# Performance work log

Hardware: AMD Instinct MI355X
Metric: run time of the kernel (lower is better)

## Reference

```python
import jax, jax.numpy as jnp
import numpy as np

B, S, D = 4, 2048, 2048
E = 8
H = (4 * D) // E  # per-expert hidden = 1024
DS = D // 2       # shared-layer hidden
LOAD_BALANCE_WEIGHT = 0.01


def setup_inputs() -> dict:
    key = jax.random.key(0)
    ks = jax.random.split(key, 12)
    s = 0.02
    return {
        "x": jax.random.normal(ks[0], (B, S, D), dtype=jnp.float32),
        "W_router": jax.random.normal(ks[1], (D, E), dtype=jnp.float32) * s,
        "b_router": jnp.zeros((E,), dtype=jnp.float32),
        "W1": jax.random.normal(ks[2], (E, D, H), dtype=jnp.float32) * s,
        "b1": jnp.zeros((E, H), dtype=jnp.float32),
        "W2": jax.random.normal(ks[3], (E, H, D), dtype=jnp.float32) * s,
        "b2": jnp.zeros((E, D), dtype=jnp.float32),
        "Ws1": jax.random.normal(ks[4], (D, DS), dtype=jnp.float32) * s,
        "bs1": jnp.zeros((DS,), dtype=jnp.float32),
        "Ws2": jax.random.normal(ks[5], (DS, D), dtype=jnp.float32) * s,
        "bs2": jnp.zeros((D,), dtype=jnp.float32),
    }


def reference(x, W_router, b_router, W1, b1, W2, b2, Ws1, bs1, Ws2, bs2):
    # Router: soft weights over all experts (soft-MoE, every expert runs).
    router_logits = jnp.einsum("bsd,de->bse", x, W_router) + b_router
    router_weights = jax.nn.softmax(router_logits, axis=-1)  # (B,S,E)

    # Shared branch: Linear -> GELU (exact, matching torch default) -> Linear.
    shared = jax.nn.gelu(jnp.einsum("bsd,dh->bsh", x, Ws1) + bs1, approximate=False)
    shared = jnp.einsum("bsh,hd->bsd", shared, Ws2) + bs2

    # All experts as one batched GEMM pair (fuses the torch Python loop).
    h = jax.nn.gelu(jnp.einsum("bsd,edh->bseh", x, W1) + b1, approximate=False)  # (B,S,E,H)
    expert_out = jnp.einsum("bseh,ehd->bsed", h, W2) + b2  # (B,S,E,D)

    # Softmax-weighted combine + scaled shared residual (dropout=0 / eval).
    weighted = jnp.einsum("bsed,bse->bsd", expert_out, router_weights)
    output = weighted + 0.1 * shared

    # Load-balance aux loss: MSE between mean usage and uniform.
    expert_usage = router_weights.mean(axis=(0, 1))  # (E,)
    uniform = jnp.full_like(expert_usage, 1.0 / E)
    aux_loss = jnp.mean((expert_usage - uniform) ** 2) * LOAD_BALANCE_WEIGHT
    return output, aux_loss
```

## Files before the change

kernel.cpp:

```cpp
#include <hip/hip_runtime.h>
#include <hip/hip_bf16.h>
#include <stdint.h>

#define DEV static __device__ __forceinline__

typedef __attribute__((ext_vector_type(4))) float f32x4;
typedef __attribute__((ext_vector_type(8))) short bf16x8;
typedef __attribute__((ext_vector_type(4))) float float4v;

constexpr int NBATCH = 4;
constexpr int SEQ    = 2048;
constexpr int DIM    = 2048;
constexpr int NEXP   = 8;
constexpr int HEXP   = 1024;
constexpr int DSH    = 1024;
constexpr int NTOK   = NBATCH * SEQ;
constexpr int JEXP   = NEXP * HEXP;
constexpr int JTOT   = JEXP + DSH;

DEV short f2bf(float f) {
  __hip_bfloat16 b = __float2bfloat16(f);
  union { __hip_bfloat16 b; short s; } u; u.b = b; return u.s;
}

DEV void gload16(const void* gp, const void* lp) {
  __builtin_amdgcn_global_load_lds(
      (__attribute__((address_space(1))) void*)(uintptr_t)gp,
      (__attribute__((address_space(3))) void*)(uint32_t)(uintptr_t)lp,
      16, 0, 0);
}

__global__ void conv_x_k(const float* __restrict__ x, short* __restrict__ xb) {
  size_t i = (size_t)blockIdx.x * blockDim.x + threadIdx.x;
  const float4v* s = reinterpret_cast<const float4v*>(x) + i * 2;
  float4v a = s[0], b = s[1];
  bf16x8 o;
  o[0] = f2bf(a.x); o[1] = f2bf(a.y); o[2] = f2bf(a.z); o[3] = f2bf(a.w);
  o[4] = f2bf(b.x); o[5] = f2bf(b.y); o[6] = f2bf(b.z); o[7] = f2bf(b.w);
  *reinterpret_cast<bf16x8*>(xb + i * 8) = o;
}

__global__ __launch_bounds__(256) void router_k(
    const float* __restrict__ x, const float* __restrict__ Wr,
    const float* __restrict__ br, float* __restrict__ rw,
    float* __restrict__ auxs) {
  const int wave = threadIdx.x >> 6, lane = threadIdx.x & 63;
  const int t = blockIdx.x * 4 + wave;
  const float* xr = x + (size_t)t * DIM;
  float a[NEXP];
#pragma unroll
  for (int e = 0; e < NEXP; ++e) a[e] = 0.f;
  for (int i = 0; i < DIM / 64; ++i) {
    int k = i * 64 + lane;
    float xv = xr[k];
    const float* w = Wr + (size_t)k * NEXP;
#pragma unroll
    for (int e = 0; e < NEXP; ++e) a[e] = fmaf(xv, w[e], a[e]);
  }
#pragma unroll
  for (int e = 0; e < NEXP; ++e) {
    float v = a[e];
#pragma unroll
    for (int off = 32; off > 0; off >>= 1) v += __shfl_xor(v, off, 64);
    a[e] = v + br[e];
  }
  float mx = a[0];
#pragma unroll
  for (int e = 1; e < NEXP; ++e) mx = fmaxf(mx, a[e]);
  float s = 0.f;
#pragma unroll
  for (int e = 0; e < NEXP; ++e) { a[e] = expf(a[e] - mx); s += a[e]; }
  float inv = 1.f / s;
#pragma unroll
  for (int e = 0; e < NEXP; ++e) a[e] *= inv;
  if (lane == 0) {
#pragma unroll
    for (int e = 0; e < NEXP; ++e) rw[(size_t)t * NEXP + e] = a[e];
  }
  __shared__ float blk[NEXP];
  if (threadIdx.x < NEXP) blk[threadIdx.x] = 0.f;
  __syncthreads();
  if (lane == 0) {
#pragma unroll
    for (int e = 0; e < NEXP; ++e) atomicAdd(&blk[e], a[e]);
  }
  __syncthreads();
  if (threadIdx.x < NEXP) atomicAdd(&auxs[threadIdx.x], blk[threadIdx.x]);
}

__global__ void zero_aux_k(float* auxs) {
  if (threadIdx.x < NEXP) auxs[threadIdx.x] = 0.f;
}

__global__ void fin_aux_k(const float* __restrict__ auxs, float* __restrict__ dst) {
  if (threadIdx.x == 0) {
    float s = 0.f;
    for (int e = 0; e < NEXP; ++e) {
      float u = auxs[e] / (float)NTOK - (1.0f / NEXP);
      s += u * u;
    }
    dst[0] = (s / NEXP) * 0.01f;
  }
}

__global__ __launch_bounds__(256) void conv_w1_k(
    const float* __restrict__ W1, const float* __restrict__ Ws1,
    short* __restrict__ dst, int jbase, int jc) {
  __shared__ float tile[64][65];
  const int j0 = jbase + blockIdx.x * 64;
  const int k0 = blockIdx.y * 64;
  const int tx = threadIdx.x & 63;
  const int ty = threadIdx.x >> 6;
#pragma unroll
  for (int i = 0; i < 16; ++i) {
    int kk = ty * 16 + i;
    int j = j0 + tx, k = k0 + kk;
    float v;
    if (j < JEXP) {
      int e = j >> 10, h = j & 1023;
      v = W1[(size_t)e * DIM * HEXP + (size_t)k * HEXP + h];
    } else {
      v = Ws1[(size_t)k * DSH + (j - JEXP)];
    }
    tile[kk][tx] = v;
  }
  __syncthreads();
#pragma unroll
  for (int i = 0; i < 16; ++i) {
    int jj = ty * 16 + i;
    int jloc = j0 - jbase + jj;
    dst[(size_t)jloc * DIM + k0 + tx] = f2bf(tile[tx][jj]);
  }
}

__global__ __launch_bounds__(256) void conv_w2_k(
    const float* __restrict__ W2, const float* __restrict__ Ws2,
    short* __restrict__ dst, int jbase, int jc) {
  __shared__ float tile[64][65];
  const int j0 = jbase + blockIdx.x * 64;
  const int d0 = blockIdx.y * 64;
  const int tx = threadIdx.x & 63;
  const int ty = threadIdx.x >> 6;
#pragma unroll
  for (int i = 0; i < 16; ++i) {
    int jj = ty * 16 + i;
    int j = j0 + jj;
    float v;
    if (j < JEXP) {
      int e = j >> 10, h = j & 1023;
      v = W2[(size_t)e * HEXP * DIM + (size_t)h * DIM + d0 + tx];
    } else {
      v = 0.1f * Ws2[(size_t)(j - JEXP) * DIM + d0 + tx];
    }
    tile[jj][tx] = v;
  }
  __syncthreads();
#pragma unroll
  for (int i = 0; i < 16; ++i) {
    int dd = ty * 16 + i;
    dst[(size_t)(d0 + dd) * jc + (j0 - jbase) + tx] = f2bf(tile[tx][dd]);
  }
}

#define MF_ROW(MI, AV)                                                           \
  acc[MI][0] = __builtin_amdgcn_mfma_f32_16x16x32_bf16(AV, b0, acc[MI][0], 0, 0, 0); \
  acc[MI][1] = __builtin_amdgcn_mfma_f32_16x16x32_bf16(AV, b1, acc[MI][1], 0, 0, 0); \
  acc[MI][2] = __builtin_amdgcn_mfma_f32_16x16x32_bf16(AV, b2, acc[MI][2], 0, 0, 0); \
  acc[MI][3] = __builtin_amdgcn_mfma_f32_16x16x32_bf16(AV, b3, acc[MI][3], 0, 0, 0);

template <int MODE>
__global__ __launch_bounds__(512, 2) void gemm256(
    const short* __restrict__ A, const short* __restrict__ Bt, int K,
    const float* __restrict__ rw,
    const float* __restrict__ bias_a, const float* __restrict__ bias_b,
    short* __restrict__ hOut, int jbase, int jc,
    float* __restrict__ out, int nx) {
  extern __shared__ short smem[];
  short* As = smem;
  short* Bs = smem + 32768;

  const int tid = threadIdx.x;
  const int w = tid >> 6, lane = tid & 63;
  const int wr = w >> 2, wc = w & 3;

  const int nwg = nx * (NTOK / 256);
  int orig = blockIdx.x;
  const int q = nwg >> 3, r = nwg & 7;
  const int xcd = orig & 7, off = orig >> 3;
  const int bid = (xcd < r ? xcd * (q + 1) : r * (q + 1) + (xcd - r) * q) + off;
  const int bx = bid % nx, by = bid / nx;
  const int m0 = by * 256, n0 = bx * 256;

  f32x4 acc[8][4] = {};

  const int aoff = ((lane & 15) << 6) + ((((lane >> 4) ^ ((lane >> 1) & 3)) & 3) << 4);
  const char* Abase = (const char*)As + wr * 8192 + aoff;
  const char* Bbase = (const char*)Bs + wc * 4096 + aoff;

  const int srow = lane >> 2;
  const int scol = (((lane & 3) ^ ((lane >> 3) & 3)) << 3);
  const short* gA0 = A + (size_t)(m0 + w * 32 + srow) * K + scol;
  const short* gB0 = Bt + (size_t)(n0 + w * 32 + srow) * K + scol;
  const size_t k16 = (size_t)16 * K;
  short* lA = As + w * 1024;
  short* lB = Bs + w * 1024;
  const int NT = K >> 5;

#define STG_A(TT) { const int sl_ = (TT) & 3; const size_t co_ = (size_t)(TT) << 5; \
    gload16(gA0 + co_, lA + sl_ * 8192);                                           \
    gload16(gA0 + k16 + co_, lA + sl_ * 8192 + 512); }
#define STG_B(TT) { const int sl_ = (TT) & 3; const size_t co_ = (size_t)(TT) << 5; \
    gload16(gB0 + co_, lB + sl_ * 8192);                                           \
    gload16(gB0 + k16 + co_, lB + sl_ * 8192 + 512); }

  STG_A(0); STG_B(0); STG_A(1); STG_B(1); STG_A(2); STG_B(2);
  asm volatile("s_waitcnt vmcnt(8)" ::: "memory");
  __builtin_amdgcn_s_barrier();

  for (int t = 0; t < NT; ++t) {
    const char* pa = Abase + (size_t)(t & 3) * 16384;
    const char* pb = Bbase + (size_t)(t & 3) * 16384;
    bf16x8 b0 = *(const bf16x8*)(pb);
    bf16x8 b1 = *(const bf16x8*)(pb + 1024);
    bf16x8 b2 = *(const bf16x8*)(pb + 2048);
    bf16x8 b3 = *(const bf16x8*)(pb + 3072);
    bf16x8 a0 = *(const bf16x8*)(pa);
    bf16x8 a1 = *(const bf16x8*)(pa + 1024);
    bf16x8 a2 = *(const bf16x8*)(pa + 2048);
    bf16x8 a3 = *(const bf16x8*)(pa + 3072);
    if (t + 3 < NT) STG_A(t + 3);
    __builtin_amdgcn_s_barrier();
    asm volatile("s_waitcnt lgkmcnt(0)" ::: "memory");
    __builtin_amdgcn_sched_barrier(0);
    __builtin_amdgcn_s_setprio(1);
    MF_ROW(0, a0) MF_ROW(1, a1) MF_ROW(2, a2) MF_ROW(3, a3)
    __builtin_amdgcn_s_setprio(0);
    __builtin_amdgcn_s_barrier();
    a0 = *(const bf16x8*)(pa + 4096);
    a1 = *(const bf16x8*)(pa + 5120);
    a2 = *(const bf16x8*)(pa + 6144);
    a3 = *(const bf16x8*)(pa + 7168);
    if (t + 3 < NT) STG_B(t + 3);
    __builtin_amdgcn_s_barrier();
    asm volatile("s_waitcnt lgkmcnt(0)" ::: "memory");
    __builtin_amdgcn_sched_barrier(0);
    __builtin_amdgcn_s_setprio(1);
    MF_ROW(4, a0) MF_ROW(5, a1) MF_ROW(6, a2) MF_ROW(7, a3)
    __builtin_amdgcn_s_setprio(0);
    if (t <= NT - 4)      { asm volatile("s_waitcnt vmcnt(8)" ::: "memory"); }
    else if (t == NT - 3) { asm volatile("s_waitcnt vmcnt(4)" ::: "memory"); }
    else if (t == NT - 2) { asm volatile("s_waitcnt vmcnt(0)" ::: "memory"); }
    __builtin_amdgcn_s_barrier();
  }
#undef STG_A
#undef STG_B

  const int r0 = (lane >> 4) * 4;
  const int ccol = lane & 15;
#pragma unroll
  for (int m = 0; m < 8; ++m) {
#pragma unroll
    for (int i = 0; i < 4; ++i) {
      const int trow = m0 + wr * 128 + m * 16 + r0 + i;
      if (MODE == 0) {
#pragma unroll
        for (int n = 0; n < 4; ++n) {
          const int col = n0 + wc * 64 + n * 16 + ccol;
          const int j = jbase + col;
          float v = acc[m][n][i];
          float bias = (j < JEXP) ? bias_a[j] : bias_b[j - JEXP];
          float val = v + bias;
          float g = 0.5f * val * (1.0f + erff(val * 0.70710678118654752f));
          float wgt = (j < JEXP) ? rw[(size_t)trow * NEXP + (j >> 10)] : 1.0f;
          hOut[(size_t)trow * jc + col] = f2bf(g * wgt);
        }
      } else if (MODE == 1) {
        float rw8[8];
#pragma unroll
        for (int e = 0; e < 8; ++e) rw8[e] = rw[(size_t)trow * NEXP + e];
#pragma unroll
        for (int n = 0; n < 4; ++n) {
          const int col = n0 + wc * 64 + n * 16 + ccol;
          float bias = 0.1f * bias_b[col];
#pragma unroll
          for (int e = 0; e < 8; ++e) bias += rw8[e] * bias_a[(size_t)e * DIM + col];
          out[(size_t)trow * DIM + col] = acc[m][n][i] + bias;
        }
      } else {
#pragma unroll
        for (int n = 0; n < 4; ++n) {
          const int col = n0 + wc * 64 + n * 16 + ccol;
          out[(size_t)trow * DIM + col] += acc[m][n][i];
        }
      }
    }
  }
}

template <int MODE>
__global__ __launch_bounds__(256) void gemm128(
    const short* __restrict__ A, const short* __restrict__ Bt, int K,
    const float* __restrict__ rw,
    const float* __restrict__ bias_a, const float* __restrict__ bias_b,
    short* __restrict__ hOut, int jbase, int jc,
    float* __restrict__ out) {
  __shared__ short As[128 * 64];
  __shared__ short Bs[128 * 64];
  const int tid = threadIdx.x;
  const int wave = tid >> 6, lane = tid & 63;
  const int wr = wave >> 1, wc = wave & 1;
  const int m0 = blockIdx.y * 128;
  const int n0 = blockIdx.x * 128;

  f32x4 acc[4][4] = {};

  const int srow = wave * 8 + (lane >> 3);
  const int scol = (((lane & 7) ^ (lane >> 3)) << 3);
  const short* gA = A + (size_t)(m0 + srow) * K + scol;
  const short* gB = Bt + (size_t)(n0 + srow) * K + scol;
  const short* lA = As + wave * 512;
  const short* lB = Bs + wave * 512;

  const int rrow = lane & 15;
  const int koff = lane >> 4;
  const int kxor = lane & 7;

  for (int kt = 0; kt < K; kt += 64) {
#pragma unroll
    for (int i = 0; i < 4; ++i) {
      gload16(gA + (size_t)i * 32 * K + kt, lA + i * 2048);
      gload16(gB + (size_t)i * 32 * K + kt, lB + i * 2048);
    }
    asm volatile("s_waitcnt vmcnt(0)" ::: "memory");
    __syncthreads();
#pragma unroll
    for (int kk = 0; kk < 2; ++kk) {
      bf16x8 af[4], bfv[4];
#pragma unroll
      for (int m = 0; m < 4; ++m) {
        int row = wr * 64 + m * 16 + rrow;
        int chunk = (kk * 4 + koff) ^ kxor;
        af[m] = *reinterpret_cast<const bf16x8*>(&As[row * 64 + chunk * 8]);
      }
#pragma unroll
      for (int n = 0; n < 4; ++n) {
        int row = wc * 64 + n * 16 + rrow;
        int chunk = (kk * 4 + koff) ^ kxor;
        bfv[n] = *reinterpret_cast<const bf16x8*>(&Bs[row * 64 + chunk * 8]);
      }
#pragma unroll
      for (int m = 0; m < 4; ++m)
#pragma unroll
        for (int n = 0; n < 4; ++n)
          acc[m][n] = __builtin_amdgcn_mfma_f32_16x16x32_bf16(af[m], bfv[n], acc[m][n], 0, 0, 0);
    }
    __syncthreads();
  }

  const int r0 = (lane >> 4) * 4;
  const int ccol = lane & 15;
#pragma unroll
  for (int m = 0; m < 4; ++m) {
#pragma unroll
    for (int n = 0; n < 4; ++n) {
      int col = n0 + wc * 64 + n * 16 + ccol;
#pragma unroll
      for (int i = 0; i < 4; ++i) {
        int t = m0 + wr * 64 + m * 16 + r0 + i;
        float v = acc[m][n][i];
        if (MODE == 0) {
          int j = jbase + col;
          float bias = (j < JEXP) ? bias_a[j] : bias_b[j - JEXP];
          float val = v + bias;
          float g = 0.5f * val * (1.0f + erff(val * 0.70710678118654752f));
          float wg = (j < JEXP) ? rw[(size_t)t * NEXP + (j >> 10)] : 1.0f;
          hOut[(size_t)t * jc + col] = f2bf(g * wg);
        } else if (MODE == 1) {
          float bias = 0.1f * bias_b[col];
#pragma unroll
          for (int e = 0; e < NEXP; ++e)
            bias += rw[(size_t)t * NEXP + e] * bias_a[(size_t)e * DIM + col];
          out[(size_t)t * DIM + col] = v + bias;
        } else {
          out[(size_t)t * DIM + col] += v;
        }
      }
    }
  }
}

extern "C" void kernel_launch(void* const* d_in, const int* in_sizes, int n_in,
                              void* d_out, int out_size, void* d_ws, size_t ws_size,
                              hipStream_t stream) {
  const float* x   = (const float*)d_in[0];
  const float* Wr  = (const float*)d_in[1];
  const float* br  = (const float*)d_in[2];
  const float* W1  = (const float*)d_in[3];
  const float* b1  = (const float*)d_in[4];
  const float* W2  = (const float*)d_in[5];
  const float* b2  = (const float*)d_in[6];
  const float* Ws1 = (const float*)d_in[7];
  const float* bs1 = (const float*)d_in[8];
  const float* Ws2 = (const float*)d_in[9];
  const float* bs2 = (const float*)d_in[10];
  float* out = (float*)d_out;

  char* wsb = (char*)d_ws;
  short* xb   = (short*)wsb;
  float* rw   = (float*)(wsb + 33554432);
  float* auxs = (float*)(wsb + 33816576);
  const size_t need_fixed = 33816832ull;

  const int jcands[8] = {9216, 4608, 3072, 2304, 1536, 768, 512, 256};
  int jc = 256;
  for (int ci = 0; ci < 8; ++ci) {
    if (need_fixed + (size_t)jcands[ci] * 24576ull <= ws_size) { jc = jcands[ci]; break; }
  }
  const int nc = JTOT / jc;
  short* w1t  = (short*)(wsb + need_fixed);
  short* w2t  = w1t + (size_t)jc * DIM;
  short* hbuf = w2t + (size_t)DIM * jc;

  bool big = true;
  {
    auto* f0 = gemm256<0>; auto* f1 = gemm256<1>; auto* f2 = gemm256<2>;
    if (hipFuncSetAttribute(reinterpret_cast<const void*>(f0),
                            hipFuncAttributeMaxDynamicSharedMemorySize, 131072) != hipSuccess) big = false;
    if (hipFuncSetAttribute(reinterpret_cast<const void*>(f1),
                            hipFuncAttributeMaxDynamicSharedMemorySize, 131072) != hipSuccess) big = false;
    if (hipFuncSetAttribute(reinterpret_cast<const void*>(f2),
                            hipFuncAttributeMaxDynamicSharedMemorySize, 131072) != hipSuccess) big = false;
  }

  zero_aux_k<<<1, 64, 0, stream>>>(auxs);
  conv_x_k<<<(NTOK * DIM / 8) / 256, 256, 0, stream>>>(x, xb);
  router_k<<<NTOK / 4, 256, 0, stream>>>(x, Wr, br, rw, auxs);
  fin_aux_k<<<1, 64, 0, stream>>>(auxs, out + (size_t)NTOK * DIM);

  for (int c = 0; c < nc; ++c) {
    const int jbase = c * jc;
    conv_w1_k<<<dim3(jc / 64, DIM / 64), 256, 0, stream>>>(W1, Ws1, w1t, jbase, jc);
    conv_w2_k<<<dim3(jc / 64, DIM / 64), 256, 0, stream>>>(W2, Ws2, w2t, jbase, jc);
    if (big) {
      const int nx1 = jc / 256, ny = NTOK / 256;
      gemm256<0><<<nx1 * ny, 512, 131072, stream>>>(
          xb, w1t, DIM, rw, b1, bs1, hbuf, jbase, jc, nullptr, nx1);
      const int nx2 = DIM / 256;
      if (c == 0) {
        gemm256<1><<<nx2 * ny, 512, 131072, stream>>>(
            hbuf, w2t, jc, rw, b2, bs2, nullptr, 0, jc, out, nx2);
      } else {
        gemm256<2><<<nx2 * ny, 512, 131072, stream>>>(
            hbuf, w2t, jc, rw, nullptr, nullptr, nullptr, 0, jc, out, nx2);
      }
    } else {
      gemm128<0><<<dim3(jc / 128, NTOK / 128), 256, 0, stream>>>(
          xb, w1t, DIM, rw, b1, bs1, hbuf, jbase, jc, nullptr);
      if (c == 0) {
        gemm128<1><<<dim3(DIM / 128, NTOK / 128), 256, 0, stream>>>(
            hbuf, w2t, jc, rw, b2, bs2, nullptr, 0, jc, out);
      } else {
        gemm128<2><<<dim3(DIM / 128, NTOK / 128), 256, 0, stream>>>(
            hbuf, w2t, jc, rw, nullptr, nullptr, nullptr, 0, jc, out);
      }
    }
  }
}
```

Measured before the change: 977.2 us.

## Software-pipeline LDS fragment loads across iterations and cut per-iteration barriers

```diff
diff --git a/kernel.cpp b/kernel.cpp
--- a/kernel.cpp
+++ b/kernel.cpp
@@ -161,12 +161,6 @@
     dst[(size_t)(d0 + dd) * jc + (j0 - jbase) + tx] = f2bf(tile[tx][dd]);
   }
 }
-
-#define MF_ROW(MI, AV)                                                           \
-  acc[MI][0] = __builtin_amdgcn_mfma_f32_16x16x32_bf16(AV, b0, acc[MI][0], 0, 0, 0); \
-  acc[MI][1] = __builtin_amdgcn_mfma_f32_16x16x32_bf16(AV, b1, acc[MI][1], 0, 0, 0); \
-  acc[MI][2] = __builtin_amdgcn_mfma_f32_16x16x32_bf16(AV, b2, acc[MI][2], 0, 0, 0); \
-  acc[MI][3] = __builtin_amdgcn_mfma_f32_16x16x32_bf16(AV, b3, acc[MI][3], 0, 0, 0);
 
 template <int MODE>
 __global__ __launch_bounds__(512, 2) void gemm256(
@@ -216,41 +210,54 @@
   STG_A(0); STG_B(0); STG_A(1); STG_B(1); STG_A(2); STG_B(2);
   asm volatile("s_waitcnt vmcnt(8)" ::: "memory");
   __builtin_amdgcn_s_barrier();
+  __builtin_amdgcn_sched_barrier(0);
+
+  bf16x8 bc[4], a03[4], a47[4], bn[4], a03n[4];
+#pragma unroll
+  for (int i = 0; i < 4; ++i) bc[i]  = *(const bf16x8*)(Bbase + i * 1024);
+#pragma unroll
+  for (int i = 0; i < 4; ++i) a03[i] = *(const bf16x8*)(Abase + i * 1024);
 
   for (int t = 0; t < NT; ++t) {
     const char* pa = Abase + (size_t)(t & 3) * 16384;
-    const char* pb = Bbase + (size_t)(t & 3) * 16384;
-    bf16x8 b0 = *(const bf16x8*)(pb);
-    bf16x8 b1 = *(const bf16x8*)(pb + 1024);
-    bf16x8 b2 = *(const bf16x8*)(pb + 2048);
-    bf16x8 b3 = *(const bf16x8*)(pb + 3072);
-    bf16x8 a0 = *(const bf16x8*)(pa);
-    bf16x8 a1 = *(const bf16x8*)(pa + 1024);
-    bf16x8 a2 = *(const bf16x8*)(pa + 2048);
-    bf16x8 a3 = *(const bf16x8*)(pa + 3072);
+#pragma unroll
+    for (int i = 0; i < 4; ++i) a47[i] = *(const bf16x8*)(pa + 4096 + i * 1024);
+    if (t <= NT - 3) { asm volatile("s_waitcnt vmcnt(4)" ::: "memory"); }
+    else             { asm volatile("s_waitcnt vmcnt(0)" ::: "memory"); }
+    __builtin_amdgcn_s_barrier();
+    __builtin_amdgcn_sched_barrier(0);
     if (t + 3 < NT) STG_A(t + 3);
-    __builtin_amdgcn_s_barrier();
-    asm volatile("s_waitcnt lgkmcnt(0)" ::: "memory");
+    asm volatile("s_waitcnt lgkmcnt(4)" ::: "memory");
     __builtin_amdgcn_sched_barrier(0);
     __builtin_amdgcn_s_setprio(1);
-    MF_ROW(0, a0) MF_ROW(1, a1) MF_ROW(2, a2) MF_ROW(3, a3)
+#pragma unroll
+    for (int mi = 0; mi < 4; ++mi)
+#pragma unroll
+      for (int ni = 0; ni < 4; ++ni)
+        acc[mi][ni] = __builtin_amdgcn_mfma_f32_16x16x32_bf16(a03[mi], bc[ni], acc[mi][ni], 0, 0, 0);
     __builtin_amdgcn_s_setprio(0);
-    __builtin_amdgcn_s_barrier();
-    a0 = *(const bf16x8*)(pa + 4096);
-    a1 = *(const bf16x8*)(pa + 5120);
-    a2 = *(const bf16x8*)(pa + 6144);
-    a3 = *(const bf16x8*)(pa + 7168);
-    if (t + 3 < NT) STG_B(t + 3);
-    __builtin_amdgcn_s_barrier();
-    asm volatile("s_waitcnt lgkmcnt(0)" ::: "memory");
+    if (t + 1 < NT) {
+      const char* pan = Abase + (size_t)((t + 1) & 3) * 16384;
+      const char* pbn = Bbase + (size_t)((t + 1) & 3) * 16384;
+#pragma unroll
+      for (int i = 0; i < 4; ++i) bn[i]   = *(const bf16x8*)(pbn + i * 1024);
+#pragma unroll
+      for (int i = 0; i < 4; ++i) a03n[i] = *(const bf16x8*)(pan + i * 1024);
+      if (t + 3 < NT) STG_B(t + 3);
+      asm volatile("s_waitcnt lgkmcnt(8)" ::: "memory");
+    } else {
+      asm volatile("s_waitcnt lgkmcnt(0)" ::: "memory");
+    }
     __builtin_amdgcn_sched_barrier(0);
     __builtin_amdgcn_s_setprio(1);
-    MF_ROW(4, a0) MF_ROW(5, a1) MF_ROW(6, a2) MF_ROW(7, a3)
+#pragma unroll
+    for (int mi = 0; mi < 4; ++mi)
+#pragma unroll
+      for (int ni = 0; ni < 4; ++ni)
+        acc[mi + 4][ni] = __builtin_amdgcn_mfma_f32_16x16x32_bf16(a47[mi], bc[ni], acc[mi + 4][ni], 0, 0, 0);
     __builtin_amdgcn_s_setprio(0);
-    if (t <= NT - 4)      { asm volatile("s_waitcnt vmcnt(8)" ::: "memory"); }
-    else if (t == NT - 3) { asm volatile("s_waitcnt vmcnt(4)" ::: "memory"); }
-    else if (t == NT - 2) { asm volatile("s_waitcnt vmcnt(0)" ::: "memory"); }
-    __builtin_amdgcn_s_barrier();
+#pragma unroll
+    for (int i = 0; i < 4; ++i) { bc[i] = bn[i]; a03[i] = a03n[i]; }
   }
 #undef STG_A
 #undef STG_B
```

Result: faster. 940.2 us (-3.8%).
